# Kernel optimization log

Measured on AMD Instinct MI355X. Metric: run time of the kernel, lower is better.

## Reference

```python
import jax, jax.numpy as jnp
import numpy as np

B, T, C = 2, 2048, 1024
NH, HS = 16, 64  # n_heads, head_size; NH*HS == C


def setup_inputs() -> dict:
    key = jax.random.key(0)
    k1, k2, k3 = jax.random.split(key, 3)
    x = jax.random.normal(k1, (B, T, C), dtype=jnp.float32)
    W_attn = jax.random.normal(k2, (C, 3 * C), dtype=jnp.float32) * (C ** -0.5)
    b_attn = jax.random.normal(k3, (3 * C,), dtype=jnp.float32) * 0.02
    return {"x": x, "W_attn": W_attn, "b_attn": b_attn}


def reference(x, W_attn, b_attn):
    Bv, Tv, Cv = x.shape
    qkv = x @ W_attn + b_attn                       # [B,T,3C]
    q, k, v = jnp.split(qkv, 3, axis=-1)            # each [B,T,C]
    q = q.reshape(Bv, Tv, NH, HS)
    k = k.reshape(Bv, Tv, NH, HS)
    v = v.reshape(Bv, Tv, NH, HS)
    scale = HS ** -0.5
    wei = jnp.einsum('bqhd,bkhd->bhqk', q, k) * scale  # [B,H,T,T]
    causal = jnp.tril(jnp.ones((Tv, Tv), dtype=bool))
    wei = jnp.where(causal[None, None], wei, -jnp.inf)
    wei = jax.nn.softmax(wei, axis=-1)
    # dropout layers are identity in eval mode
    out = jnp.einsum('bhqk,bkhd->bqhd', wei, v)     # [B,T,H,HS]
    return out.reshape(Bv, Tv, Cv)
```

## Files before the change

### kernel.cpp

```cpp
#include <hip/hip_runtime.h>
#include <hip/hip_bf16.h>
#include <math.h>

#define BB   2
#define TT   2048
#define CC   1024
#define NH   16
#define HS   64
#define N3C  3072
#define MM   4096

typedef __attribute__((ext_vector_type(8))) short bf16x8;
typedef __attribute__((ext_vector_type(4))) float f32x4;

#define NINF (-__builtin_inff())
#define QSCALE 0.125f

__device__ __forceinline__ unsigned short f2bf(float f) {
    unsigned int u = __builtin_bit_cast(unsigned int, f);
    unsigned int r = u + 0x7fffu + ((u >> 16) & 1u);
    return (unsigned short)(r >> 16);
}

__device__ __forceinline__ unsigned short f2bf_fast(float f) {
    unsigned int u = __builtin_bit_cast(unsigned int, f);
    return (unsigned short)((u + 0x8000u) >> 16);
}

__device__ __forceinline__ void gl_lds16(const unsigned short* g, unsigned short* l) {
    __builtin_amdgcn_global_load_lds(
        (const __attribute__((address_space(1))) unsigned int*)g,
        (__attribute__((address_space(3))) unsigned int*)l, 16, 0, 0);
}

__global__ __launch_bounds__(256) void k_cast(const float* __restrict__ x,
                                              unsigned short* __restrict__ xb) {
    int i = (blockIdx.x * 256 + threadIdx.x) * 4;
    float4 v = *(const float4*)(x + i);
    ushort4 o;
    o.x = f2bf(v.x); o.y = f2bf(v.y); o.z = f2bf(v.z); o.w = f2bf(v.w);
    *(ushort4*)(xb + i) = o;
}

__global__ __launch_bounds__(256) void k_transpose_w(const float* __restrict__ W,
                                                     unsigned short* __restrict__ Wt) {
    __shared__ float tile[32][33];
    const int n0 = blockIdx.x * 32;
    const int k0 = blockIdx.y * 32;
    const int t = threadIdx.x;
    {
        int kr = t >> 3, ns = (t & 7) * 4;
        float4 v = *(const float4*)(W + (size_t)(k0 + kr) * N3C + n0 + ns);
        tile[kr][ns + 0] = v.x; tile[kr][ns + 1] = v.y;
        tile[kr][ns + 2] = v.z; tile[kr][ns + 3] = v.w;
    }
    __syncthreads();
    {
        int nr = t >> 3, ks = (t & 7) * 4;
        ushort4 o;
        o.x = f2bf(tile[ks + 0][nr]);
        o.y = f2bf(tile[ks + 1][nr]);
        o.z = f2bf(tile[ks + 2][nr]);
        o.w = f2bf(tile[ks + 3][nr]);
        *(ushort4*)(Wt + (size_t)(n0 + nr) * CC + k0 + ks) = o;
    }
}

#define EPS 72

__global__ __launch_bounds__(256) void k_gemm_qkv(const unsigned short* __restrict__ xb,
                                                  const unsigned short* __restrict__ wt,
                                                  const float* __restrict__ bias,
                                                  unsigned short* __restrict__ qb,
                                                  unsigned short* __restrict__ kb,
                                                  unsigned short* __restrict__ vt) {
    __shared__ unsigned short sA[128 * 32];
    __shared__ unsigned short sB[128 * 32];
    __shared__ unsigned short sE[4 * 64 * EPS];
    const int t = threadIdx.x;
    const int wave = t >> 6, lane = t & 63;
    const int quad = lane >> 4, c16 = lane & 15;
    const int wm = wave >> 1, wn = wave & 1;
    const int m0 = blockIdx.y * 128;
    const int n0 = blockIdx.x * 128;
    const int sel = n0 >> 10;

    f32x4 acc[4][4];
#pragma unroll
    for (int i = 0; i < 4; ++i)
#pragma unroll
        for (int j = 0; j < 4; ++j) acc[i][j] = f32x4{0, 0, 0, 0};

    const int srow = wave * 16 + (lane >> 2);
    const int scol = (lane & 3) * 8;
    const unsigned short* gA = xb + (size_t)(m0 + srow) * CC + scol;
    const unsigned short* gB = wt + (size_t)(n0 + srow) * CC + scol;
    unsigned short* lA = sA + wave * 512 + lane * 8;
    unsigned short* lB = sB + wave * 512 + lane * 8;

    for (int k0 = 0; k0 < CC; k0 += 32) {
        __syncthreads();
        gl_lds16(gA + k0, lA);
        gl_lds16(gA + k0 + (size_t)64 * CC, lA + 2048);
        gl_lds16(gB + k0, lB);
        gl_lds16(gB + k0 + (size_t)64 * CC, lB + 2048);
        __syncthreads();
        bf16x8 a[4], b[4];
#pragma unroll
        for (int rt = 0; rt < 4; ++rt)
            a[rt] = *(const bf16x8*)(sA + (wm * 64 + rt * 16 + c16) * 32 + quad * 8);
#pragma unroll
        for (int ct = 0; ct < 4; ++ct)
            b[ct] = *(const bf16x8*)(sB + (wn * 64 + ct * 16 + c16) * 32 + quad * 8);
#pragma unroll
        for (int rt = 0; rt < 4; ++rt)
#pragma unroll
            for (int ct = 0; ct < 4; ++ct)
                acc[rt][ct] = __builtin_amdgcn_mfma_f32_16x16x32_bf16(b[ct], a[rt], acc[rt][ct], 0, 0, 0);
    }

    const int head = ((n0 + wn * 64) >> 6) & 15;
    const int bh = (m0 >> 11) * NH + head;
    const int tbase = (m0 & 2047) + wm * 64;
    if (sel < 2) {
        unsigned short* dst = (sel == 0) ? qb : kb;
        const float sc = (sel == 0) ? QSCALE : 1.0f;
        unsigned short* ew = sE + wave * (64 * EPS);
#pragma unroll
        for (int ct = 0; ct < 4; ++ct) {
            const float4 bv4 = *(const float4*)(bias + n0 + wn * 64 + ct * 16 + quad * 4);
            const int d0 = ct * 16 + quad * 4;
#pragma unroll
            for (int rt = 0; rt < 4; ++rt) {
                ushort4 pk;
                pk.x = f2bf((acc[rt][ct][0] + bv4.x) * sc);
                pk.y = f2bf((acc[rt][ct][1] + bv4.y) * sc);
                pk.z = f2bf((acc[rt][ct][2] + bv4.z) * sc);
                pk.w = f2bf((acc[rt][ct][3] + bv4.w) * sc);
                *(ushort4*)(ew + (rt * 16 + c16) * EPS + d0) = pk;
            }
        }
        const size_t gbase = ((size_t)bh * TT + tbase) * HS;
#pragma unroll
        for (int i = 0; i < 8; ++i) {
            const int trow = i * 8 + (lane >> 3);
            bf16x8 row = *(const bf16x8*)(ew + trow * EPS + (lane & 7) * 8);
            *(bf16x8*)(dst + gbase + (size_t)trow * HS + (lane & 7) * 8) = row;
        }
    } else {
#pragma unroll
        for (int ct = 0; ct < 4; ++ct) {
            const float4 bv4 = *(const float4*)(bias + n0 + wn * 64 + ct * 16 + quad * 4);
#pragma unroll
            for (int r = 0; r < 4; ++r) {
                const int d = ct * 16 + quad * 4 + r;
                const float bv = ((const float*)&bv4)[r];
#pragma unroll
                for (int rt = 0; rt < 4; ++rt) {
                    const int tt = tbase + rt * 16 + c16;
                    vt[((size_t)bh * HS + d) * TT + tt] = f2bf(acc[rt][ct][r] + bv);
                }
            }
        }
    }
}

#define SPP 72
#define AW  4

__global__ __launch_bounds__(256) void k_attn(const unsigned short* __restrict__ qb,
                                              const unsigned short* __restrict__ kb,
                                              const unsigned short* __restrict__ vt,
                                              float* __restrict__ out) {
    __shared__ unsigned short sK[2][64 * 64];
    __shared__ unsigned short sV[2][64 * 64];
    __shared__ unsigned short sP[AW][32 * SPP];

    const int tid = threadIdx.x;
    const int wave = tid >> 6, lane = tid & 63;
    const int quad = lane >> 4, c16 = lane & 15;
    const int g = blockIdx.x >> 5;
    const int qbk = 15 - g;
    const int bh = blockIdx.x & 31;
    const int qw = qbk * 128 + wave * 32;
    const int qmax = qw + 31;
    const int kiters = 2 * (qbk + 1);

    const unsigned short* Qp = qb + (size_t)bh * TT * HS;
    const unsigned short* Kp = kb + (size_t)bh * TT * HS;
    const unsigned short* Vp = vt + (size_t)bh * HS * TT;

    bf16x8 qf[2][2];
#pragma unroll
    for (int j = 0; j < 2; ++j)
#pragma unroll
        for (int ks = 0; ks < 2; ++ks)
            qf[j][ks] = *(const bf16x8*)(Qp + (size_t)(qw + j * 16 + c16) * HS + ks * 32 + quad * 8);

    f32x4 o[4][2];
#pragma unroll
    for (int dt = 0; dt < 4; ++dt)
#pragma unroll
        for (int j = 0; j < 2; ++j) o[dt][j] = f32x4{0, 0, 0, 0};
    float lsum[2] = {0.f, 0.f};

    unsigned short* sPw = sP[wave];

    const int srow = tid >> 3;
    const int ssc = tid & 7;
    auto stage = [&](int buf, int kt) {
        const int kb0 = kt * 64;
#pragma unroll
        for (int rnd = 0; rnd < 2; ++rnd) {
            const int row = rnd * 32 + srow;
            const int sl = ((ssc ^ (row & 7)) * 8);
            gl_lds16(Kp + (size_t)(kb0 + row) * HS + sl, &sK[buf][rnd * 2048 + tid * 8]);
            gl_lds16(Vp + (size_t)row * TT + kb0 + sl, &sV[buf][rnd * 2048 + tid * 8]);
        }
    };

    auto tile = [&](int buf, int kt) {
        const int kb0 = kt * 64;
        const unsigned short* Kb = sK[buf];
        const unsigned short* Vb = sV[buf];
        bf16x8 kf[4][2];
#pragma unroll
        for (int mt = 0; mt < 4; ++mt)
#pragma unroll
            for (int ks = 0; ks < 2; ++ks)
                kf[mt][ks] = *(const bf16x8*)(Kb + (mt * 16 + c16) * 64 +
                                              (((ks * 4 + quad) ^ (c16 & 7)) * 8));
        f32x4 s[4][2];
#pragma unroll
        for (int mt = 0; mt < 4; ++mt)
#pragma unroll
            for (int j = 0; j < 2; ++j) s[mt][j] = f32x4{0, 0, 0, 0};
#pragma unroll
        for (int mt = 0; mt < 4; ++mt)
#pragma unroll
            for (int j = 0; j < 2; ++j) {
                s[mt][j] = __builtin_amdgcn_mfma_f32_16x16x32_bf16(kf[mt][0], qf[j][0], s[mt][j], 0, 0, 0);
                s[mt][j] = __builtin_amdgcn_mfma_f32_16x16x32_bf16(kf[mt][1], qf[j][1], s[mt][j], 0, 0, 0);
            }
        bf16x8 vf[4][2];
#pragma unroll
        for (int dt = 0; dt < 4; ++dt)
#pragma unroll
            for (int ks = 0; ks < 2; ++ks)
                vf[dt][ks] = *(const bf16x8*)(Vb + (dt * 16 + c16) * 64 +
                                              (((ks * 4 + quad) ^ (c16 & 7)) * 8));
        const bool maskit = (kb0 + 63 > qw);
#pragma unroll
        for (int j = 0; j < 2; ++j) {
            const int rowq = qw + j * 16 + c16;
            float l = 0.f;
#pragma unroll
            for (int mt = 0; mt < 4; ++mt) {
                float p0, p1, p2, p3;
                if (maskit) {
                    const int k = kb0 + mt * 16 + quad * 4;
                    p0 = __expf((k     <= rowq) ? s[mt][j][0] : NINF);
                    p1 = __expf((k + 1 <= rowq) ? s[mt][j][1] : NINF);
                    p2 = __expf((k + 2 <= rowq) ? s[mt][j][2] : NINF);
                    p3 = __expf((k + 3 <= rowq) ? s[mt][j][3] : NINF);
                } else {
                    p0 = __expf(s[mt][j][0]);
                    p1 = __expf(s[mt][j][1]);
                    p2 = __expf(s[mt][j][2]);
                    p3 = __expf(s[mt][j][3]);
                }
                l += (p0 + p1) + (p2 + p3);
                ushort4 pk;
                pk.x = f2bf_fast(p0); pk.y = f2bf_fast(p1);
                pk.z = f2bf_fast(p2); pk.w = f2bf_fast(p3);
                *(ushort4*)(sPw + (j * 16 + c16) * SPP + mt * 16 + quad * 4) = pk;
            }
            lsum[j] += l;
        }
        bf16x8 pf[2][2];
#pragma unroll
        for (int j = 0; j < 2; ++j)
#pragma unroll
            for (int ks = 0; ks < 2; ++ks)
                pf[j][ks] = *(const bf16x8*)(sPw + (j * 16 + c16) * SPP + ks * 32 + quad * 8);
#pragma unroll
        for (int dt = 0; dt < 4; ++dt)
#pragma unroll
            for (int j = 0; j < 2; ++j) {
                o[dt][j] = __builtin_amdgcn_mfma_f32_16x16x32_bf16(vf[dt][0], pf[j][0], o[dt][j], 0, 0, 0);
                o[dt][j] = __builtin_amdgcn_mfma_f32_16x16x32_bf16(vf[dt][1], pf[j][1], o[dt][j], 0, 0, 0);
            }
    };

    stage(0, 0);
    for (int kt = 0; kt < kiters; ++kt) {
        if (kt + 1 < kiters) {
            stage((kt + 1) & 1, kt + 1);
            asm volatile("s_waitcnt vmcnt(4)" ::: "memory");
        } else {
            asm volatile("s_waitcnt vmcnt(0)" ::: "memory");
        }
        __builtin_amdgcn_s_barrier();
        asm volatile("" ::: "memory");
        if (kt * 64 <= qmax) tile(kt & 1, kt);
        __builtin_amdgcn_s_barrier();
        asm volatile("" ::: "memory");
    }

#pragma unroll
    for (int j = 0; j < 2; ++j) {
        lsum[j] += __shfl_xor(lsum[j], 16);
        lsum[j] += __shfl_xor(lsum[j], 32);
    }

    const int b_ = bh >> 4, h_ = bh & 15;
#pragma unroll
    for (int j = 0; j < 2; ++j) {
        const float il = 1.0f / lsum[j];
        const int q = qw + j * 16 + c16;
        float* orow = out + ((size_t)(b_ * TT + q)) * CC + h_ * HS;
#pragma unroll
        for (int dt = 0; dt < 4; ++dt) {
            float4 w;
            w.x = o[dt][j][0] * il; w.y = o[dt][j][1] * il;
            w.z = o[dt][j][2] * il; w.w = o[dt][j][3] * il;
            *(float4*)(orow + dt * 16 + quad * 4) = w;
        }
    }
}

extern "C" void kernel_launch(void* const* d_in, const int* in_sizes, int n_in,
                              void* d_out, int out_size, void* d_ws, size_t ws_size,
                              hipStream_t stream) {
    const float* x    = (const float*)d_in[0];
    const float* W    = (const float*)d_in[1];
    const float* bias = (const float*)d_in[2];
    float* out = (float*)d_out;

    char* ws = (char*)d_ws;
    unsigned short* xb = (unsigned short*)(ws);
    unsigned short* wt = (unsigned short*)(ws + 8388608);
    unsigned short* qb = (unsigned short*)(ws + 8388608 + 6291456);
    unsigned short* kb = (unsigned short*)(ws + 8388608 + 6291456 + 8388608);
    unsigned short* vt = (unsigned short*)(ws + 8388608 + 6291456 + 2 * 8388608);

    k_cast<<<dim3(MM * CC / (256 * 4)), dim3(256), 0, stream>>>(x, xb);
    k_transpose_w<<<dim3(N3C / 32, CC / 32), dim3(256), 0, stream>>>(W, wt);
    k_gemm_qkv<<<dim3(N3C / 128, MM / 128), dim3(256), 0, stream>>>(xb, wt, bias, qb, kb, vt);
    k_attn<<<dim3(16 * 32), dim3(256), 0, stream>>>(qb, kb, vt, out);
}
```

Measured before the change: 179.2 us.

## Pair causal query blocks per workgroup and widen attention blocks to 8 waves

```diff
diff --git a/kernel.cpp b/kernel.cpp
--- a/kernel.cpp
+++ b/kernel.cpp
@@ -166,164 +166,145 @@
 }
 
 #define SPP 72
-#define AW  4
-
-__global__ __launch_bounds__(256) void k_attn(const unsigned short* __restrict__ qb,
+
+__global__ __launch_bounds__(512) void k_attn(const unsigned short* __restrict__ qb,
                                               const unsigned short* __restrict__ kb,
                                               const unsigned short* __restrict__ vt,
                                               float* __restrict__ out) {
     __shared__ unsigned short sK[2][64 * 64];
     __shared__ unsigned short sV[2][64 * 64];
-    __shared__ unsigned short sP[AW][32 * SPP];
+    __shared__ unsigned short sP[8][16 * SPP];
 
     const int tid = threadIdx.x;
     const int wave = tid >> 6, lane = tid & 63;
     const int quad = lane >> 4, c16 = lane & 15;
     const int g = blockIdx.x >> 5;
-    const int qbk = 15 - g;
     const int bh = blockIdx.x & 31;
-    const int qw = qbk * 128 + wave * 32;
-    const int qmax = qw + 31;
-    const int kiters = 2 * (qbk + 1);
 
     const unsigned short* Qp = qb + (size_t)bh * TT * HS;
     const unsigned short* Kp = kb + (size_t)bh * TT * HS;
     const unsigned short* Vp = vt + (size_t)bh * HS * TT;
 
-    bf16x8 qf[2][2];
-#pragma unroll
-    for (int j = 0; j < 2; ++j)
-#pragma unroll
-        for (int ks = 0; ks < 2; ++ks)
-            qf[j][ks] = *(const bf16x8*)(Qp + (size_t)(qw + j * 16 + c16) * HS + ks * 32 + quad * 8);
-
-    f32x4 o[4][2];
-#pragma unroll
-    for (int dt = 0; dt < 4; ++dt)
-#pragma unroll
-        for (int j = 0; j < 2; ++j) o[dt][j] = f32x4{0, 0, 0, 0};
-    float lsum[2] = {0.f, 0.f};
-
     unsigned short* sPw = sP[wave];
 
     const int srow = tid >> 3;
     const int ssc = tid & 7;
+    const int sl = (ssc ^ (srow & 7)) * 8;
+    const unsigned short* Ksrc = Kp + (size_t)srow * HS + sl;
+    const unsigned short* Vsrc = Vp + (size_t)srow * TT + sl;
     auto stage = [&](int buf, int kt) {
         const int kb0 = kt * 64;
-#pragma unroll
-        for (int rnd = 0; rnd < 2; ++rnd) {
-            const int row = rnd * 32 + srow;
-            const int sl = ((ssc ^ (row & 7)) * 8);
-            gl_lds16(Kp + (size_t)(kb0 + row) * HS + sl, &sK[buf][rnd * 2048 + tid * 8]);
-            gl_lds16(Vp + (size_t)row * TT + kb0 + sl, &sV[buf][rnd * 2048 + tid * 8]);
-        }
+        gl_lds16(Ksrc + (size_t)kb0 * HS, &sK[buf][tid * 8]);
+        gl_lds16(Vsrc + kb0, &sV[buf][tid * 8]);
     };
 
-    auto tile = [&](int buf, int kt) {
-        const int kb0 = kt * 64;
-        const unsigned short* Kb = sK[buf];
-        const unsigned short* Vb = sV[buf];
-        bf16x8 kf[4][2];
-#pragma unroll
-        for (int mt = 0; mt < 4; ++mt)
-#pragma unroll
-            for (int ks = 0; ks < 2; ++ks)
-                kf[mt][ks] = *(const bf16x8*)(Kb + (mt * 16 + c16) * 64 +
-                                              (((ks * 4 + quad) ^ (c16 & 7)) * 8));
-        f32x4 s[4][2];
-#pragma unroll
-        for (int mt = 0; mt < 4; ++mt)
-#pragma unroll
-            for (int j = 0; j < 2; ++j) s[mt][j] = f32x4{0, 0, 0, 0};
-#pragma unroll
-        for (int mt = 0; mt < 4; ++mt)
-#pragma unroll
-            for (int j = 0; j < 2; ++j) {
-                s[mt][j] = __builtin_amdgcn_mfma_f32_16x16x32_bf16(kf[mt][0], qf[j][0], s[mt][j], 0, 0, 0);
-                s[mt][j] = __builtin_amdgcn_mfma_f32_16x16x32_bf16(kf[mt][1], qf[j][1], s[mt][j], 0, 0, 0);
-            }
-        bf16x8 vf[4][2];
-#pragma unroll
-        for (int dt = 0; dt < 4; ++dt)
-#pragma unroll
-            for (int ks = 0; ks < 2; ++ks)
-                vf[dt][ks] = *(const bf16x8*)(Vb + (dt * 16 + c16) * 64 +
-                                              (((ks * 4 + quad) ^ (c16 & 7)) * 8));
-        const bool maskit = (kb0 + 63 > qw);
-#pragma unroll
-        for (int j = 0; j < 2; ++j) {
-            const int rowq = qw + j * 16 + c16;
+    const int b_ = bh >> 4, h_ = bh & 15;
+
+#pragma unroll 1
+    for (int ph = 0; ph < 2; ++ph) {
+        const int p = ph ? g : (15 - g);
+        const int qw = p * 128 + wave * 16;
+        const int qmax = qw + 15;
+        const int kiters = 2 * p + 2;
+
+        bf16x8 qf[2];
+#pragma unroll
+        for (int ks = 0; ks < 2; ++ks)
+            qf[ks] = *(const bf16x8*)(Qp + (size_t)(qw + c16) * HS + ks * 32 + quad * 8);
+
+        f32x4 o[4];
+#pragma unroll
+        for (int dt = 0; dt < 4; ++dt) o[dt] = f32x4{0, 0, 0, 0};
+        float lsum = 0.f;
+
+        auto tile = [&](int buf, int kt) {
+            const int kb0 = kt * 64;
+            const unsigned short* Kb = sK[buf];
+            const unsigned short* Vb = sV[buf];
+            bf16x8 kf[4][2];
+#pragma unroll
+            for (int mt = 0; mt < 4; ++mt)
+#pragma unroll
+                for (int ks = 0; ks < 2; ++ks)
+                    kf[mt][ks] = *(const bf16x8*)(Kb + (mt * 16 + c16) * 64 +
+                                                  (((ks * 4 + quad) ^ (c16 & 7)) * 8));
+            f32x4 s[4];
+#pragma unroll
+            for (int mt = 0; mt < 4; ++mt) s[mt] = f32x4{0, 0, 0, 0};
+#pragma unroll
+            for (int mt = 0; mt < 4; ++mt) {
+                s[mt] = __builtin_amdgcn_mfma_f32_16x16x32_bf16(kf[mt][0], qf[0], s[mt], 0, 0, 0);
+                s[mt] = __builtin_amdgcn_mfma_f32_16x16x32_bf16(kf[mt][1], qf[1], s[mt], 0, 0, 0);
+            }
+            bf16x8 vf[4][2];
+#pragma unroll
+            for (int dt = 0; dt < 4; ++dt)
+#pragma unroll
+                for (int ks = 0; ks < 2; ++ks)
+                    vf[dt][ks] = *(const bf16x8*)(Vb + (dt * 16 + c16) * 64 +
+                                                  (((ks * 4 + quad) ^ (c16 & 7)) * 8));
+            const bool maskit = (kb0 + 63 > qw);
+            const int rowq = qw + c16;
             float l = 0.f;
 #pragma unroll
             for (int mt = 0; mt < 4; ++mt) {
                 float p0, p1, p2, p3;
                 if (maskit) {
                     const int k = kb0 + mt * 16 + quad * 4;
-                    p0 = __expf((k     <= rowq) ? s[mt][j][0] : NINF);
-                    p1 = __expf((k + 1 <= rowq) ? s[mt][j][1] : NINF);
-                    p2 = __expf((k + 2 <= rowq) ? s[mt][j][2] : NINF);
-                    p3 = __expf((k + 3 <= rowq) ? s[mt][j][3] : NINF);
+                    p0 = __expf((k     <= rowq) ? s[mt][0] : NINF);
+                    p1 = __expf((k + 1 <= rowq) ? s[mt][1] : NINF);
+                    p2 = __expf((k + 2 <= rowq) ? s[mt][2] : NINF);
+                    p3 = __expf((k + 3 <= rowq) ? s[mt][3] : NINF);
                 } else {
-                    p0 = __expf(s[mt][j][0]);
-                    p1 = __expf(s[mt][j][1]);
-                    p2 = __expf(s[mt][j][2]);
-                    p3 = __expf(s[mt][j][3]);
+                    p0 = __expf(s[mt][0]);
+                    p1 = __expf(s[mt][1]);
+                    p2 = __expf(s[mt][2]);
+                    p3 = __expf(s[mt][3]);
                 }
                 l += (p0 + p1) + (p2 + p3);
                 ushort4 pk;
                 pk.x = f2bf_fast(p0); pk.y = f2bf_fast(p1);
                 pk.z = f2bf_fast(p2); pk.w = f2bf_fast(p3);
-                *(ushort4*)(sPw + (j * 16 + c16) * SPP + mt * 16 + quad * 4) = pk;
-            }
-            lsum[j] += l;
-        }
-        bf16x8 pf[2][2];
-#pragma unroll
-        for (int j = 0; j < 2; ++j)
+                *(ushort4*)(sPw + c16 * SPP + mt * 16 + quad * 4) = pk;
+            }
+            lsum += l;
+            bf16x8 pf[2];
 #pragma unroll
             for (int ks = 0; ks < 2; ++ks)
-                pf[j][ks] = *(const bf16x8*)(sPw + (j * 16 + c16) * SPP + ks * 32 + quad * 8);
-#pragma unroll
-        for (int dt = 0; dt < 4; ++dt)
-#pragma unroll
-            for (int j = 0; j < 2; ++j) {
-                o[dt][j] = __builtin_amdgcn_mfma_f32_16x16x32_bf16(vf[dt][0], pf[j][0], o[dt][j], 0, 0, 0);
-                o[dt][j] = __builtin_amdgcn_mfma_f32_16x16x32_bf16(vf[dt][1], pf[j][1], o[dt][j], 0, 0, 0);
-            }
-    };
-
-    stage(0, 0);
-    for (int kt = 0; kt < kiters; ++kt) {
-        if (kt + 1 < kiters) {
-            stage((kt + 1) & 1, kt + 1);
-            asm volatile("s_waitcnt vmcnt(4)" ::: "memory");
-        } else {
-            asm volatile("s_waitcnt vmcnt(0)" ::: "memory");
-        }
-        __builtin_amdgcn_s_barrier();
-        asm volatile("" ::: "memory");
-        if (kt * 64 <= qmax) tile(kt & 1, kt);
-        __builtin_amdgcn_s_barrier();
-        asm volatile("" ::: "memory");
-    }
-
-#pragma unroll
-    for (int j = 0; j < 2; ++j) {
-        lsum[j] += __shfl_xor(lsum[j], 16);
-        lsum[j] += __shfl_xor(lsum[j], 32);
-    }
-
-    const int b_ = bh >> 4, h_ = bh & 15;
-#pragma unroll
-    for (int j = 0; j < 2; ++j) {
-        const float il = 1.0f / lsum[j];
-        const int q = qw + j * 16 + c16;
+                pf[ks] = *(const bf16x8*)(sPw + c16 * SPP + ks * 32 + quad * 8);
+#pragma unroll
+            for (int dt = 0; dt < 4; ++dt) {
+                o[dt] = __builtin_amdgcn_mfma_f32_16x16x32_bf16(vf[dt][0], pf[0], o[dt], 0, 0, 0);
+                o[dt] = __builtin_amdgcn_mfma_f32_16x16x32_bf16(vf[dt][1], pf[1], o[dt], 0, 0, 0);
+            }
+        };
+
+        stage(0, 0);
+        for (int kt = 0; kt < kiters; ++kt) {
+            if (kt + 1 < kiters) {
+                stage((kt + 1) & 1, kt + 1);
+                asm volatile("s_waitcnt vmcnt(2)" ::: "memory");
+            } else {
+                asm volatile("s_waitcnt vmcnt(0)" ::: "memory");
+            }
+            __builtin_amdgcn_s_barrier();
+            asm volatile("" ::: "memory");
+            if (kt * 64 <= qmax) tile(kt & 1, kt);
+            __builtin_amdgcn_s_barrier();
+            asm volatile("" ::: "memory");
+        }
+
+        lsum += __shfl_xor(lsum, 16);
+        lsum += __shfl_xor(lsum, 32);
+
+        const float il = 1.0f / lsum;
+        const int q = qw + c16;
         float* orow = out + ((size_t)(b_ * TT + q)) * CC + h_ * HS;
 #pragma unroll
         for (int dt = 0; dt < 4; ++dt) {
             float4 w;
-            w.x = o[dt][j][0] * il; w.y = o[dt][j][1] * il;
-            w.z = o[dt][j][2] * il; w.w = o[dt][j][3] * il;
+            w.x = o[dt][0] * il; w.y = o[dt][1] * il;
+            w.z = o[dt][2] * il; w.w = o[dt][3] * il;
             *(float4*)(orow + dt * 16 + quad * 4) = w;
         }
     }
@@ -347,5 +328,5 @@
     k_cast<<<dim3(MM * CC / (256 * 4)), dim3(256), 0, stream>>>(x, xb);
     k_transpose_w<<<dim3(N3C / 32, CC / 32), dim3(256), 0, stream>>>(W, wt);
     k_gemm_qkv<<<dim3(N3C / 128, MM / 128), dim3(256), 0, stream>>>(xb, wt, bias, qb, kb, vt);
-    k_attn<<<dim3(16 * 32), dim3(256), 0, stream>>>(qb, kb, vt, out);
-}
+    k_attn<<<dim3(8 * 32), dim3(512), 0, stream>>>(qb, kb, vt, out);
+}
```

After: 168.3 us. 1.06x faster.
